# Performance work log

Measured on AMD Instinct MI355X. Metric: run time of the kernel, lower is better.

## Reference

```python
import jax, jax.numpy as jnp
import numpy as np

B, N_PER, C, KG, KTOP, KNN = 8, 2048, 256, 16, 512, 32
N = B * N_PER
E = N * KG
EPS = 1e-5


def setup_inputs() -> dict:
    key = jax.random.key(0)
    ks = jax.random.split(key, 32)
    s = 0.05
    x = jax.random.normal(ks[0], (N, C), jnp.float32)
    x_origin = jax.random.normal(ks[1], (N, C), jnp.float32)
    xyz = jax.random.uniform(ks[2], (N, 3), jnp.float32)
    # graph: every node is a dst with KG incoming edges from random nodes of the SAME sample
    edge_dst = jnp.repeat(jnp.arange(N, dtype=jnp.int32), KG)
    src_local = jax.random.randint(ks[3], (E,), 0, N_PER, dtype=jnp.int32)
    edge_src = src_local + (edge_dst // N_PER) * N_PER
    # EdgeConv params (theta on x_j - x_i, phi on x_i)
    theta_w = jax.random.normal(ks[4], (C, C), jnp.float32) * s
    theta_b = jax.random.normal(ks[5], (C,), jnp.float32) * s
    phi_w = jax.random.normal(ks[6], (C, C), jnp.float32) * s
    phi_b = jax.random.normal(ks[7], (C,), jnp.float32) * s
    # region_score_mlp: Conv1d(C,64,1)-ReLU-BN(64)-Conv1d(64,32,1)-ReLU-BN(32)-Conv1d(32,1,1)
    w1 = jax.random.normal(ks[8], (64, C), jnp.float32) * s
    b1 = jax.random.normal(ks[9], (64,), jnp.float32) * s
    g1 = 1.0 + 0.1 * jax.random.normal(ks[10], (64,), jnp.float32)
    be1 = 0.1 * jax.random.normal(ks[11], (64,), jnp.float32)
    m1 = 0.1 * jax.random.normal(ks[12], (64,), jnp.float32)
    v1 = jax.random.uniform(ks[13], (64,), jnp.float32, 0.5, 1.5)
    w2 = jax.random.normal(ks[14], (32, 64), jnp.float32) * s
    b2 = jax.random.normal(ks[15], (32,), jnp.float32) * s
    g2 = 1.0 + 0.1 * jax.random.normal(ks[16], (32,), jnp.float32)
    be2 = 0.1 * jax.random.normal(ks[17], (32,), jnp.float32)
    m2 = 0.1 * jax.random.normal(ks[18], (32,), jnp.float32)
    v2 = jax.random.uniform(ks[19], (32,), jnp.float32, 0.5, 1.5)
    w3 = jax.random.normal(ks[20], (1, 32), jnp.float32) * s
    b3 = jax.random.normal(ks[21], (1,), jnp.float32) * s
    return dict(x=x, x_origin=x_origin, xyz=xyz, edge_src=edge_src, edge_dst=edge_dst,
                theta_w=theta_w, theta_b=theta_b, phi_w=phi_w, phi_b=phi_b,
                w1=w1, b1=b1, g1=g1, be1=be1, m1=m1, v1=v1,
                w2=w2, b2=b2, g2=g2, be2=be2, m2=m2, v2=v2, w3=w3, b3=b3)


def _bn(t, g, b, m, v):
    return (t - m) * jax.lax.rsqrt(v + EPS) * g + b


def _forward(x, x_origin, xyz, edge_src, edge_dst,
             theta_w, theta_b, phi_w, phi_b,
             w1, b1, g1, be1, m1, v1, w2, b2, g2, be2, m2, v2, w3, b3):
    # EdgeConv: h_i = max_{j->i}( theta(x_j - x_i) + phi(x_i) ), then residual add
    msg = ((x[edge_src] - x[edge_dst]) @ theta_w.T + theta_b
           + x[edge_dst] @ phi_w.T + phi_b)                      # [E, C]
    h = jax.ops.segment_max(msg, edge_dst, num_segments=N)       # [N, C]
    x1 = h + x                                                   # residual
    # per-node MLP (Conv1d kernel-size 1 == linear), BN in eval mode
    t = _bn(jax.nn.relu(x1 @ w1.T + b1), g1, be1, m1, v1)
    t = _bn(jax.nn.relu(t @ w2.T + b2), g2, be2, m2, v2)
    score = t @ w3.T + b3                                        # [N, 1]
    score_b = score.reshape(B, N_PER)                            # vps_score
    # per-batch top-k (cls=False path: select by raw score, descending)
    topk_vals, topk_idx = jax.lax.top_k(score_b, KTOP)           # [B, KTOP]
    perm = (topk_idx + jnp.arange(B, dtype=topk_idx.dtype)[:, None] * N_PER).reshape(-1)
    x_new = x1[perm].reshape(B, KTOP, C)
    x_copy = x_origin[perm].reshape(B, KTOP, -1)
    xyz_sel = xyz[perm].reshape(B, KTOP, 3)
    # rebuild 32-NN graph per sample on selected points (batched, no per-b python calls)
    d2 = jnp.sum((xyz_sel[:, :, None, :] - xyz_sel[:, None, :, :]) ** 2, axis=-1)  # [B,K,K]
    _, knn_idx = jax.lax.top_k(-d2, KNN)                         # [B, KTOP, 32]
    return knn_idx, x_new, x_copy, score_b, topk_vals


def reference(x, x_origin, xyz, edge_src, edge_dst,
              theta_w, theta_b, phi_w, phi_b,
              w1, b1, g1, be1, m1, v1, w2, b2, g2, be2, m2, v2, w3, b3):
    return _forward(x, x_origin, xyz, edge_src, edge_dst,
                    theta_w, theta_b, phi_w, phi_b,
                    w1, b1, g1, be1, m1, v1, w2, b2, g2, be2, m2, v2, w3, b3)
```

## Files before the change

kernel.cpp:

```cpp
#include <hip/hip_runtime.h>
#include <math.h>

constexpr int B     = 8;
constexpr int N_PER = 2048;
constexpr int C     = 256;
constexpr int KG    = 16;
constexpr int KTOP  = 512;
constexpr int KNN   = 32;
constexpr int N     = B * N_PER;
constexpr float EPS = 1e-5f;

typedef __attribute__((ext_vector_type(8))) short  short8;
typedef __attribute__((ext_vector_type(4))) float  f32x4;

__device__ inline void split3(float f, unsigned short& h, unsigned short& m,
                              unsigned short& l)
{
    const unsigned u  = __float_as_uint(f);
    const unsigned r1 = (u + 0x7FFFu + ((u >> 16) & 1u)) & 0xFFFF0000u;
    h = (unsigned short)(r1 >> 16);
    const float f2 = f - __uint_as_float(r1);
    const unsigned u2 = __float_as_uint(f2);
    const unsigned r2 = (u2 + 0x7FFFu + ((u2 >> 16) & 1u)) & 0xFFFF0000u;
    m = (unsigned short)(r2 >> 16);
    const float f3 = f2 - __uint_as_float(r2);
    const unsigned u3 = __float_as_uint(f3);
    l = (unsigned short)((u3 + 0x7FFFu + ((u3 >> 16) & 1u)) >> 16);
}

__device__ inline void cvt_store24(unsigned short* dh, unsigned short* dm,
                                   unsigned short* dl, float4 a, float4 b)
{
    short8 h, m, l;
    unsigned short hh, mm, ll;
    float v[8] = {a.x, a.y, a.z, a.w, b.x, b.y, b.z, b.w};
#pragma unroll
    for (int j = 0; j < 8; ++j) {
        split3(v[j], hh, mm, ll);
        h[j] = (short)hh;
        m[j] = (short)mm;
        l[j] = (short)ll;
    }
    *(short8*)dh = h;
    *(short8*)dm = m;
    *(short8*)dl = l;
}

__device__ inline void split8v(const float* __restrict__ s,
                               unsigned short* __restrict__ dh,
                               unsigned short* __restrict__ dm,
                               unsigned short* __restrict__ dl)
{
    float4 a = *(const float4*)s;
    float4 b = *(const float4*)(s + 4);
    float v[8] = {a.x, a.y, a.z, a.w, b.x, b.y, b.z, b.w};
    short8 h8, m8, l8;
    unsigned short hh, mm, ll;
#pragma unroll
    for (int j = 0; j < 8; ++j) {
        split3(v[j], hh, mm, ll);
        h8[j] = (short)hh;
        m8[j] = (short)mm;
        l8[j] = (short)ll;
    }
    *(short8*)dh = h8;
    *(short8*)dm = m8;
    *(short8*)dl = l8;
}

constexpr int GW = C * C / 8;

__global__ __launch_bounds__(256) void k0w_split(
    const float* __restrict__ thw, const float* __restrict__ phw,
    unsigned short* __restrict__ th, unsigned short* __restrict__ tm,
    unsigned short* __restrict__ tl,
    unsigned short* __restrict__ ph, unsigned short* __restrict__ pm,
    unsigned short* __restrict__ pl)
{
    const int g = blockIdx.x * 256 + threadIdx.x;
    if (g < GW) {
        const int o = g * 8;
        split8v(thw + o, th + o, tm + o, tl + o);
    } else if (g < 2 * GW) {
        const int o = (g - GW) * 8;
        split8v(phw + o, ph + o, pm + o, pl + o);
    }
}

__global__ __launch_bounds__(256) void k1_wp(
    const float* __restrict__ x,
    const unsigned short* __restrict__ th, const unsigned short* __restrict__ tm,
    const unsigned short* __restrict__ tl,
    const unsigned short* __restrict__ ph, const unsigned short* __restrict__ pm,
    const unsigned short* __restrict__ pl,
    const float* __restrict__ thb, const float* __restrict__ phb,
    float* __restrict__ T, float* __restrict__ R)
{
    constexpr int BM = 128, BN = 64, ST = 40;
    __shared__ unsigned short sA[3][BM * ST];
    __shared__ unsigned short sT[3][BN * ST];
    __shared__ unsigned short sP[3][BN * ST];

    const int tid  = threadIdx.x;
    const int row0 = blockIdx.x * BM;
    const int n0   = blockIdx.y * BN;
    const int lane = tid & 63;
    const int wv   = tid >> 6;
    const int wr   = (wv >> 1) * 64;
    const int wc   = (wv & 1) * 32;
    const int fr   = lane & 15;
    const int fk   = (lane >> 4) * 8;
    const int ar0  = tid >> 2;
    const int ac   = (tid & 3) * 8;

    f32x4 acTh[4][2], acTl[4][2], acQh[4][2], acQl[4][2];
    const f32x4 zz = {0.f, 0.f, 0.f, 0.f};
#pragma unroll
    for (int m = 0; m < 4; ++m)
#pragma unroll
        for (int n = 0; n < 2; ++n) {
            acTh[m][n] = zz; acTl[m][n] = zz;
            acQh[m][n] = zz; acQl[m][n] = zz;
        }

    const float* xA0 = x + (size_t)(row0 + ar0)      * C + ac;
    const float* xA1 = x + (size_t)(row0 + 64 + ar0) * C + ac;
    const size_t offW = (size_t)(n0 + ar0) * C + ac;

    float4 a0a = *(const float4*)(xA0 + 0), a0b = *(const float4*)(xA0 + 4);
    float4 a1a = *(const float4*)(xA1 + 0), a1b = *(const float4*)(xA1 + 4);
    short8 rTh = *(const short8*)(th + offW);
    short8 rTm = *(const short8*)(tm + offW);
    short8 rTl = *(const short8*)(tl + offW);
    short8 rPh = *(const short8*)(ph + offW);
    short8 rPm = *(const short8*)(pm + offW);
    short8 rPl = *(const short8*)(pl + offW);

    const int sOffA0 = ar0 * ST + ac;
    const int sOffA1 = (64 + ar0) * ST + ac;
    const int aBase  = (wr + fr) * ST + fk;
    const int bBase  = (wc + fr) * ST + fk;

    for (int step = 0; step < 8; ++step) {
        __syncthreads();
        cvt_store24(sA[0] + sOffA0, sA[1] + sOffA0, sA[2] + sOffA0, a0a, a0b);
        cvt_store24(sA[0] + sOffA1, sA[1] + sOffA1, sA[2] + sOffA1, a1a, a1b);
        *(short8*)(sT[0] + sOffA0) = rTh;
        *(short8*)(sT[1] + sOffA0) = rTm;
        *(short8*)(sT[2] + sOffA0) = rTl;
        *(short8*)(sP[0] + sOffA0) = rPh;
        *(short8*)(sP[1] + sOffA0) = rPm;
        *(short8*)(sP[2] + sOffA0) = rPl;
        __syncthreads();

        if (step < 7) {
            const int kn = (step + 1) * 32;
            a0a = *(const float4*)(xA0 + kn); a0b = *(const float4*)(xA0 + kn + 4);
            a1a = *(const float4*)(xA1 + kn); a1b = *(const float4*)(xA1 + kn + 4);
            rTh = *(const short8*)(th + offW + kn);
            rTm = *(const short8*)(tm + offW + kn);
            rTl = *(const short8*)(tl + offW + kn);
            rPh = *(const short8*)(ph + offW + kn);
            rPm = *(const short8*)(pm + offW + kn);
            rPl = *(const short8*)(pl + offW + kn);
        }

        short8 a1f[4], a2f[4], a3f[4];
#pragma unroll
        for (int m = 0; m < 4; ++m) {
            const int r = aBase + m * 16 * ST;
            a1f[m] = *(const short8*)(sA[0] + r);
            a2f[m] = *(const short8*)(sA[1] + r);
            a3f[m] = *(const short8*)(sA[2] + r);
        }
        {
            short8 t0[2], p0[2];
#pragma unroll
            for (int n = 0; n < 2; ++n) {
                const int r = bBase + n * 16 * ST;
                t0[n] = *(const short8*)(sT[0] + r);
                p0[n] = *(const short8*)(sP[0] + r);
            }
#pragma unroll
            for (int m = 0; m < 4; ++m)
#pragma unroll
                for (int n = 0; n < 2; ++n) {
                    acTh[m][n] = __builtin_amdgcn_mfma_f32_16x16x32_bf16(a1f[m], t0[n], acTh[m][n], 0, 0, 0);
                    acQh[m][n] = __builtin_amdgcn_mfma_f32_16x16x32_bf16(a1f[m], p0[n], acQh[m][n], 0, 0, 0);
                    acTl[m][n] = __builtin_amdgcn_mfma_f32_16x16x32_bf16(a2f[m], t0[n], acTl[m][n], 0, 0, 0);
                    acQl[m][n] = __builtin_amdgcn_mfma_f32_16x16x32_bf16(a2f[m], p0[n], acQl[m][n], 0, 0, 0);
                    acTl[m][n] = __builtin_amdgcn_mfma_f32_16x16x32_bf16(a3f[m], t0[n], acTl[m][n], 0, 0, 0);
                    acQl[m][n] = __builtin_amdgcn_mfma_f32_16x16x32_bf16(a3f[m], p0[n], acQl[m][n], 0, 0, 0);
                }
        }
        {
            short8 t1[2], p1[2];
#pragma unroll
            for (int n = 0; n < 2; ++n) {
                const int r = bBase + n * 16 * ST;
                t1[n] = *(const short8*)(sT[1] + r);
                p1[n] = *(const short8*)(sP[1] + r);
            }
#pragma unroll
            for (int m = 0; m < 4; ++m)
#pragma unroll
                for (int n = 0; n < 2; ++n) {
                    acTl[m][n] = __builtin_amdgcn_mfma_f32_16x16x32_bf16(a1f[m], t1[n], acTl[m][n], 0, 0, 0);
                    acQl[m][n] = __builtin_amdgcn_mfma_f32_16x16x32_bf16(a1f[m], p1[n], acQl[m][n], 0, 0, 0);
                    acTl[m][n] = __builtin_amdgcn_mfma_f32_16x16x32_bf16(a2f[m], t1[n], acTl[m][n], 0, 0, 0);
                    acQl[m][n] = __builtin_amdgcn_mfma_f32_16x16x32_bf16(a2f[m], p1[n], acQl[m][n], 0, 0, 0);
                }
        }
        {
            short8 t2[2], p2[2];
#pragma unroll
            for (int n = 0; n < 2; ++n) {
                const int r = bBase + n * 16 * ST;
                t2[n] = *(const short8*)(sT[2] + r);
                p2[n] = *(const short8*)(sP[2] + r);
            }
#pragma unroll
            for (int m = 0; m < 4; ++m)
#pragma unroll
                for (int n = 0; n < 2; ++n) {
                    acTl[m][n] = __builtin_amdgcn_mfma_f32_16x16x32_bf16(a1f[m], t2[n], acTl[m][n], 0, 0, 0);
                    acQl[m][n] = __builtin_amdgcn_mfma_f32_16x16x32_bf16(a1f[m], p2[n], acQl[m][n], 0, 0, 0);
                }
        }
    }

    const int cr = (lane >> 4) * 4;
#pragma unroll
    for (int m = 0; m < 4; ++m) {
#pragma unroll
        for (int n = 0; n < 2; ++n) {
            const int col  = n0 + wc + n * 16 + fr;
            const float bias = thb[col] + phb[col];
#pragma unroll
            for (int j = 0; j < 4; ++j) {
                const int row = row0 + wr + m * 16 + cr + j;
                const size_t off = (size_t)row * C + col;
                const float tval = acTh[m][n][j] + acTl[m][n][j];
                const float qval = acQh[m][n][j] + acQl[m][n][j];
                T[off] = tval;
                R[off] = x[off] + qval + bias - tval;
            }
        }
    }
}

__global__ __launch_bounds__(256) void k1_fb(
    const float* __restrict__ x, const float* __restrict__ thw,
    const float* __restrict__ phw, const float* __restrict__ thb,
    const float* __restrict__ phb, float* __restrict__ T, float* __restrict__ R)
{
    constexpr int BM = 128, BN = 64, ST = 40;
    __shared__ unsigned short sA[3][BM * ST];
    __shared__ unsigned short sT[3][BN * ST];
    __shared__ unsigned short sP[3][BN * ST];

    const int tid  = threadIdx.x;
    const int row0 = blockIdx.x * BM;
    const int n0   = blockIdx.y * BN;
    const int lane = tid & 63;
    const int wv   = tid >> 6;
    const int wr   = (wv >> 1) * 64;
    const int wc   = (wv & 1) * 32;
    const int fr   = lane & 15;
    const int fk   = (lane >> 4) * 8;
    const int ar0 = tid >> 2;
    const int ac  = (tid & 3) * 8;

    f32x4 acTh[4][2], acTl[4][2], acQh[4][2], acQl[4][2];
    const f32x4 zz = {0.f, 0.f, 0.f, 0.f};
#pragma unroll
    for (int m = 0; m < 4; ++m)
#pragma unroll
        for (int n = 0; n < 2; ++n) {
            acTh[m][n] = zz; acTl[m][n] = zz;
            acQh[m][n] = zz; acQl[m][n] = zz;
        }

    const float* xA0 = x   + (size_t)(row0 + ar0)      * C + ac;
    const float* xA1 = x   + (size_t)(row0 + 64 + ar0) * C + ac;
    const float* wT  = thw + (size_t)(n0 + ar0)        * C + ac;
    const float* wP  = phw + (size_t)(n0 + ar0)        * C + ac;

    float4 a0a = *(const float4*)(xA0 + 0), a0b = *(const float4*)(xA0 + 4);
    float4 a1a = *(const float4*)(xA1 + 0), a1b = *(const float4*)(xA1 + 4);
    float4 ta  = *(const float4*)(wT  + 0), tb_ = *(const float4*)(wT  + 4);
    float4 pa  = *(const float4*)(wP  + 0), pb_ = *(const float4*)(wP  + 4);

    const int sOffA0 = ar0 * ST + ac;
    const int sOffA1 = (64 + ar0) * ST + ac;
    const int aBase  = (wr + fr) * ST + fk;
    const int bBase  = (wc + fr) * ST + fk;

    for (int step = 0; step < 8; ++step) {
        __syncthreads();
        cvt_store24(sA[0] + sOffA0, sA[1] + sOffA0, sA[2] + sOffA0, a0a, a0b);
        cvt_store24(sA[0] + sOffA1, sA[1] + sOffA1, sA[2] + sOffA1, a1a, a1b);
        cvt_store24(sT[0] + sOffA0, sT[1] + sOffA0, sT[2] + sOffA0, ta,  tb_);
        cvt_store24(sP[0] + sOffA0, sP[1] + sOffA0, sP[2] + sOffA0, pa,  pb_);
        __syncthreads();

        if (step < 7) {
            const int kn = (step + 1) * 32;
            a0a = *(const float4*)(xA0 + kn); a0b = *(const float4*)(xA0 + kn + 4);
            a1a = *(const float4*)(xA1 + kn); a1b = *(const float4*)(xA1 + kn + 4);
            ta  = *(const float4*)(wT  + kn); tb_ = *(const float4*)(wT  + kn + 4);
            pa  = *(const float4*)(wP  + kn); pb_ = *(const float4*)(wP  + kn + 4);
        }

        short8 a1f[4], a2f[4], a3f[4];
#pragma unroll
        for (int m = 0; m < 4; ++m) {
            const int r = aBase + m * 16 * ST;
            a1f[m] = *(const short8*)(sA[0] + r);
            a2f[m] = *(const short8*)(sA[1] + r);
            a3f[m] = *(const short8*)(sA[2] + r);
        }
        {
            short8 t0[2], p0[2];
#pragma unroll
            for (int n = 0; n < 2; ++n) {
                const int r = bBase + n * 16 * ST;
                t0[n] = *(const short8*)(sT[0] + r);
                p0[n] = *(const short8*)(sP[0] + r);
            }
#pragma unroll
            for (int m = 0; m < 4; ++m)
#pragma unroll
                for (int n = 0; n < 2; ++n) {
                    acTh[m][n] = __builtin_amdgcn_mfma_f32_16x16x32_bf16(a1f[m], t0[n], acTh[m][n], 0, 0, 0);
                    acQh[m][n] = __builtin_amdgcn_mfma_f32_16x16x32_bf16(a1f[m], p0[n], acQh[m][n], 0, 0, 0);
                    acTl[m][n] = __builtin_amdgcn_mfma_f32_16x16x32_bf16(a2f[m], t0[n], acTl[m][n], 0, 0, 0);
                    acQl[m][n] = __builtin_amdgcn_mfma_f32_16x16x32_bf16(a2f[m], p0[n], acQl[m][n], 0, 0, 0);
                    acTl[m][n] = __builtin_amdgcn_mfma_f32_16x16x32_bf16(a3f[m], t0[n], acTl[m][n], 0, 0, 0);
                    acQl[m][n] = __builtin_amdgcn_mfma_f32_16x16x32_bf16(a3f[m], p0[n], acQl[m][n], 0, 0, 0);
                }
        }
        {
            short8 t1[2], p1[2];
#pragma unroll
            for (int n = 0; n < 2; ++n) {
                const int r = bBase + n * 16 * ST;
                t1[n] = *(const short8*)(sT[1] + r);
                p1[n] = *(const short8*)(sP[1] + r);
            }
#pragma unroll
            for (int m = 0; m < 4; ++m)
#pragma unroll
                for (int n = 0; n < 2; ++n) {
                    acTl[m][n] = __builtin_amdgcn_mfma_f32_16x16x32_bf16(a1f[m], t1[n], acTl[m][n], 0, 0, 0);
                    acQl[m][n] = __builtin_amdgcn_mfma_f32_16x16x32_bf16(a1f[m], p1[n], acQl[m][n], 0, 0, 0);
                    acTl[m][n] = __builtin_amdgcn_mfma_f32_16x16x32_bf16(a2f[m], t1[n], acTl[m][n], 0, 0, 0);
                    acQl[m][n] = __builtin_amdgcn_mfma_f32_16x16x32_bf16(a2f[m], p1[n], acQl[m][n], 0, 0, 0);
                }
        }
        {
            short8 t2[2], p2[2];
#pragma unroll
            for (int n = 0; n < 2; ++n) {
                const int r = bBase + n * 16 * ST;
                t2[n] = *(const short8*)(sT[2] + r);
                p2[n] = *(const short8*)(sP[2] + r);
            }
#pragma unroll
            for (int m = 0; m < 4; ++m)
#pragma unroll
                for (int n = 0; n < 2; ++n) {
                    acTl[m][n] = __builtin_amdgcn_mfma_f32_16x16x32_bf16(a1f[m], t2[n], acTl[m][n], 0, 0, 0);
                    acQl[m][n] = __builtin_amdgcn_mfma_f32_16x16x32_bf16(a1f[m], p2[n], acQl[m][n], 0, 0, 0);
                }
        }
    }

    const int cr = (lane >> 4) * 4;
#pragma unroll
    for (int m = 0; m < 4; ++m) {
#pragma unroll
        for (int n = 0; n < 2; ++n) {
            const int col  = n0 + wc + n * 16 + fr;
            const float bias = thb[col] + phb[col];
#pragma unroll
            for (int j = 0; j < 4; ++j) {
                const int row = row0 + wr + m * 16 + cr + j;
                const size_t off = (size_t)row * C + col;
                const float tval = acTh[m][n][j] + acTl[m][n][j];
                const float qval = acQh[m][n][j] + acQl[m][n][j];
                T[off] = tval;
                R[off] = x[off] + qval + bias - tval;
            }
        }
    }
}

__global__ __launch_bounds__(256) void k2a_gather_max(
    const int* __restrict__ esrc, const float* __restrict__ T, float* x1r)
{
    const int gb = blockIdx.x;
    const int b  = gb & 7;
    const int node0 = b * N_PER + (gb >> 3) * 4;
    const int t = threadIdx.x;
    __shared__ int s[4][KG];
    if (t < 64) s[t >> 4][t & 15] = esrc[(node0 + (t >> 4)) * KG + (t & 15)];
    __syncthreads();
    const int m  = t >> 6;
    const int c4 = (t & 63) * 4;
    float4 acc = make_float4(-INFINITY, -INFINITY, -INFINITY, -INFINITY);
#pragma unroll
    for (int k = 0; k < KG; ++k) {
        const float4 v = *(const float4*)&T[(size_t)s[m][k] * C + c4];
        acc.x = fmaxf(acc.x, v.x);  acc.y = fmaxf(acc.y, v.y);
        acc.z = fmaxf(acc.z, v.z);  acc.w = fmaxf(acc.w, v.w);
    }
    const size_t off = (size_t)(node0 + m) * C + c4;
    float4 r = *(const float4*)&x1r[off];
    r.x += acc.x;  r.y += acc.y;  r.z += acc.z;  r.w += acc.w;
    *(float4*)&x1r[off] = r;
}

__global__ __launch_bounds__(256) void k2bc_score(
    const float* __restrict__ x1, const float* __restrict__ w1,
    const float* __restrict__ b1, const float* __restrict__ g1,
    const float* __restrict__ be1, const float* __restrict__ m1,
    const float* __restrict__ v1,
    const float* __restrict__ w2, const float* __restrict__ b2,
    const float* __restrict__ g2, const float* __restrict__ be2,
    const float* __restrict__ m2, const float* __restrict__ v2,
    const float* __restrict__ w3, const float* __restrict__ b3,
    float* __restrict__ score_ws, float* __restrict__ out_score)
{
    constexpr int BK = 16, ST = 68;
    __shared__ float Xs[BK * ST];
    __shared__ float Ws[BK * ST];
    __shared__ float t1s[64 * 65];
    __shared__ float w2s[32 * 65];
    __shared__ float w3s[32];
    __shared__ float zs[64 * 33];
    const int tid  = threadIdx.x;
    const int row0 = blockIdx.x * 64;
    const int tx = tid & 15, ty = tid >> 4;
    const int lm = tid >> 2, lq = (tid & 3) << 2;

    float acc[4][4] = {{0.f}};
    for (int k0 = 0; k0 < C; k0 += BK) {
        float4 fx = *(const float4*)(x1 + (size_t)(row0 + lm) * C + k0 + lq);
        float4 fw = *(const float4*)(w1 + (size_t)lm * C + k0 + lq);
        __syncthreads();
        Xs[(lq + 0) * ST + lm] = fx.x;  Xs[(lq + 1) * ST + lm] = fx.y;
        Xs[(lq + 2) * ST + lm] = fx.z;  Xs[(lq + 3) * ST + lm] = fx.w;
        Ws[(lq + 0) * ST + lm] = fw.x;  Ws[(lq + 1) * ST + lm] = fw.y;
        Ws[(lq + 2) * ST + lm] = fw.z;  Ws[(lq + 3) * ST + lm] = fw.w;
        __syncthreads();
#pragma unroll
        for (int k = 0; k < BK; ++k) {
            float4 a4 = *(const float4*)&Xs[k * ST + (ty << 2)];
            float4 w4 = *(const float4*)&Ws[k * ST + (tx << 2)];
            float av[4] = {a4.x, a4.y, a4.z, a4.w};
            float wv[4] = {w4.x, w4.y, w4.z, w4.w};
#pragma unroll
            for (int i2 = 0; i2 < 4; ++i2)
#pragma unroll
                for (int j2 = 0; j2 < 4; ++j2) acc[i2][j2] += av[i2] * wv[j2];
        }
    }
    __syncthreads();
#pragma unroll
    for (int i2 = 0; i2 < 4; ++i2) {
        const int mrow = (ty << 2) + i2;
#pragma unroll
        for (int j2 = 0; j2 < 4; ++j2) {
            const int o = (tx << 2) + j2;
            float y = acc[i2][j2] + b1[o];
            y = fmaxf(y, 0.f);
            y = (y - m1[o]) * (1.0f / sqrtf(v1[o] + EPS)) * g1[o] + be1[o];
            t1s[mrow * 65 + o] = y;
        }
    }
    for (int idx = tid; idx < 2048; idx += 256)
        w2s[(idx >> 6) * 65 + (idx & 63)] = w2[idx];
    if (tid < 32) w3s[tid] = w3[tid];
    __syncthreads();

    const int o = tid & 31;
    const float inv2 = (1.0f / sqrtf(v2[o] + EPS)) * g2[o];
#pragma unroll
    for (int p = 0; p < 8; ++p) {
        const int nl = p * 8 + (tid >> 5);
        float z = 0.f;
#pragma unroll
        for (int j = 0; j < 64; ++j) z += t1s[nl * 65 + j] * w2s[o * 65 + j];
        z += b2[o];
        z = fmaxf(z, 0.f);
        z = (z - m2[o]) * inv2 + be2[o];
        zs[nl * 33 + o] = z;
    }
    __syncthreads();

    if (tid < 64) {
        float sacc = 0.f;
#pragma unroll
        for (int j = 0; j < 32; ++j) sacc += zs[tid * 33 + j] * w3s[j];
        sacc += b3[0];
        const int node = row0 + tid;
        score_ws[node]  = sacc;
        out_score[node] = sacc;
    }
}

__global__ __launch_bounds__(1024) void k3_topk(
    const float* __restrict__ score, const float* __restrict__ xyz,
    float* __restrict__ out_topk, int* __restrict__ perm,
    float* __restrict__ xsel)
{
    __shared__ unsigned long long keys[N_PER];
    const int b = blockIdx.x;
    const int t = threadIdx.x;
    for (int i = t; i < N_PER; i += 1024) {
        const float v = score[b * N_PER + i];
        unsigned u = __float_as_uint(v);
        const unsigned ua = (u & 0x80000000u) ? ~u : (u | 0x80000000u);
        const unsigned ud = ~ua;
        keys[i] = ((unsigned long long)ud << 32) | (unsigned)i;
    }
    __syncthreads();
    for (int k = 2; k <= N_PER; k <<= 1) {
        for (int j = k >> 1; j > 0; j >>= 1) {
            for (int i = t; i < N_PER; i += 1024) {
                const int ixj = i ^ j;
                if (ixj > i) {
                    const unsigned long long a = keys[i], c = keys[ixj];
                    const bool up = ((i & k) == 0);
                    if ((a > c) == up) { keys[i] = c; keys[ixj] = a; }
                }
            }
            __syncthreads();
        }
    }
    for (int r = t; r < KTOP; r += 1024) {
        const int idx = (int)(keys[r] & 0xffffffffu);
        const int g = b * N_PER + idx;
        out_topk[b * KTOP + r] = score[g];
        perm[b * KTOP + r] = g;
        xsel[(b * KTOP + r) * 3 + 0] = xyz[g * 3 + 0];
        xsel[(b * KTOP + r) * 3 + 1] = xyz[g * 3 + 1];
        xsel[(b * KTOP + r) * 3 + 2] = xyz[g * 3 + 2];
    }
}

__global__ __launch_bounds__(256) void k5_knn(
    const int* __restrict__ perm, const float* __restrict__ xsel,
    const float* __restrict__ x1, const float* __restrict__ xorig,
    float* __restrict__ out_xnew, float* __restrict__ out_xcopy,
    float* __restrict__ out_knn)
{
    constexpr int G = 4;
    __shared__ float px[KTOP], py[KTOP], pz[KTOP];
    __shared__ unsigned long long keys[G * KTOP];
    const int t  = threadIdx.x;
    const int q0 = blockIdx.x * G;
    const int b  = q0 >> 9;
    const int i0 = q0 & 511;

    for (int idx = t; idx < KTOP; idx += 256) {
        const size_t base = ((size_t)b * KTOP + idx) * 3;
        px[idx] = xsel[base + 0];
        py[idx] = xsel[base + 1];
        pz[idx] = xsel[base + 2];
    }
#pragma unroll
    for (int p = 0; p < G; ++p) {
        const int row = q0 + p;
        const int g = perm[row];
        out_xnew [(size_t)row * C + t] = x1   [(size_t)g * C + t];
        out_xcopy[(size_t)row * C + t] = xorig[(size_t)g * C + t];
    }
    __syncthreads();

    for (int w = t; w < G * KTOP; w += 256) {
        const int p = w >> 9, idx = w & 511;
        const float dx = __fsub_rn(px[i0 + p], px[idx]);
        const float dy = __fsub_rn(py[i0 + p], py[idx]);
        const float dz = __fsub_rn(pz[i0 + p], pz[idx]);
        const float d2 = __fadd_rn(__fadd_rn(__fmul_rn(dx, dx), __fmul_rn(dy, dy)),
                                   __fmul_rn(dz, dz));
        keys[w] = ((unsigned long long)__float_as_uint(d2) << 32) | (unsigned)idx;
    }
    __syncthreads();

    for (int k = 2; k <= 32; k <<= 1) {
        for (int j = k >> 1; j > 0; j >>= 1) {
            for (int i = t; i < G * KTOP; i += 256) {
                const int ixj = i ^ j;
                if (ixj > i) {
                    const int il = i & 31;
                    const unsigned long long a = keys[i], c = keys[ixj];
                    const bool up = ((il & k) == 0) || (k == 32);
                    if ((a > c) == up) { keys[i] = c; keys[ixj] = a; }
                }
            }
            __syncthreads();
        }
    }
    for (int r = 0; r < 4; ++r) {
        const int npairs = 8 >> r;
        const int total  = G * npairs * 32;
        for (int w = t; w < total; w += 256) {
            const int p  = w / (npairs * 32);
            const int rm = w - p * (npairs * 32);
            const int m  = rm >> 5, i = rm & 31;
            const int baseA = p * KTOP + m * (64 << r);
            const int baseB = baseA + (32 << r);
            const unsigned long long a = keys[baseA + i];
            const unsigned long long c = keys[baseB + 31 - i];
            keys[baseA + i] = (c < a) ? c : a;
        }
        __syncthreads();
        for (int j = 16; j > 0; j >>= 1) {
            for (int w = t; w < total; w += 256) {
                const int p  = w / (npairs * 32);
                const int rm = w - p * (npairs * 32);
                const int m  = rm >> 5, i = rm & 31;
                const int ixj = i ^ j;
                if (ixj > i) {
                    const int baseA = p * KTOP + m * (64 << r);
                    const unsigned long long a = keys[baseA + i], c = keys[baseA + ixj];
                    if (a > c) { keys[baseA + i] = c; keys[baseA + ixj] = a; }
                }
            }
            __syncthreads();
        }
    }

    if (t < G * KNN) {
        const int p = t >> 5, r = t & 31;
        out_knn[((size_t)(q0 + p)) * KNN + r] =
            (float)(unsigned)(keys[p * KTOP + r] & 0xffffffffu);
    }
}

extern "C" void kernel_launch(void* const* d_in, const int* in_sizes, int n_in,
                              void* d_out, int out_size, void* d_ws, size_t ws_size,
                              hipStream_t stream)
{
    const float* x     = (const float*)d_in[0];
    const float* xorig = (const float*)d_in[1];
    const float* xyz   = (const float*)d_in[2];
    const int*   esrc  = (const int*)d_in[3];
    const float* thw = (const float*)d_in[5];
    const float* thb = (const float*)d_in[6];
    const float* phw = (const float*)d_in[7];
    const float* phb = (const float*)d_in[8];
    const float* w1  = (const float*)d_in[9];
    const float* b1  = (const float*)d_in[10];
    const float* g1  = (const float*)d_in[11];
    const float* be1 = (const float*)d_in[12];
    const float* m1  = (const float*)d_in[13];
    const float* v1  = (const float*)d_in[14];
    const float* w2  = (const float*)d_in[15];
    const float* b2  = (const float*)d_in[16];
    const float* g2  = (const float*)d_in[17];
    const float* be2 = (const float*)d_in[18];
    const float* m2  = (const float*)d_in[19];
    const float* v2  = (const float*)d_in[20];
    const float* w3  = (const float*)d_in[21];
    const float* b3  = (const float*)d_in[22];

    float* ws   = (float*)d_ws;
    float* T    = ws;
    float* x1   = ws + (size_t)N * C;
    float* sc   = ws + 2 * (size_t)N * C;
    int*   perm = (int*)(sc + N);
    float* xsel = (float*)(perm + B * KTOP);

    unsigned short* th = (unsigned short*)(xsel + (size_t)B * KTOP * 3);
    unsigned short* tm = th + (size_t)C * C;
    unsigned short* tl = tm + (size_t)C * C;
    unsigned short* ph = tl + (size_t)C * C;
    unsigned short* pm = ph + (size_t)C * C;
    unsigned short* pl = pm + (size_t)C * C;
    const size_t ws_need = (size_t)((char*)(pl + (size_t)C * C) - (char*)ws);
    const bool planes_ok = (ws_size >= ws_need);

    float* out     = (float*)d_out;
    float* o_knn   = out;
    float* o_xnew  = o_knn + (size_t)B * KTOP * KNN;
    float* o_xcopy = o_xnew + (size_t)B * KTOP * C;
    float* o_score = o_xcopy + (size_t)B * KTOP * C;
    float* o_topk  = o_score + (size_t)B * N_PER;

    if (planes_ok) {
        k0w_split<<<(2 * GW + 255) / 256, 256, 0, stream>>>(
            thw, phw, th, tm, tl, ph, pm, pl);
        k1_wp<<<dim3(N / 128, C / 64), 256, 0, stream>>>(
            x, th, tm, tl, ph, pm, pl, thb, phb, T, x1);
    } else {
        k1_fb<<<dim3(N / 128, C / 64), 256, 0, stream>>>(x, thw, phw, thb, phb, T, x1);
    }
    k2a_gather_max<<<N / 4, 256, 0, stream>>>(esrc, T, x1);
    k2bc_score<<<N / 64, 256, 0, stream>>>(x1, w1, b1, g1, be1, m1, v1,
                                           w2, b2, g2, be2, m2, v2, w3, b3, sc, o_score);
    k3_topk<<<B, 1024, 0, stream>>>(sc, xyz, o_topk, perm, xsel);
    k5_knn<<<B * KTOP / 4, 256, 0, stream>>>(perm, xsel, x1, xorig,
                                             o_xnew, o_xcopy, o_knn);
}
```

Measured before the change: 255.3 us.

## Replace bitonic sorts with rank-counting top-k and wave-level kNN selection

The per-batch top-k bitonic sort ran on only 8 blocks of 1024 threads. It is replaced by a rank computation spread over 64 blocks: each thread counts how many keys are smaller than its own key and scatters its element directly if that rank is below KTOP. The kNN bitonic sort/merge in shared memory becomes a per-wave selection. Each lane sorts 8 candidates in registers, then 32 rounds of wave-wide shuffle min-reductions extract the nearest neighbours. This removes many __syncthreads barriers and shared-memory passes, at the cost of O(N^2) comparisons in the rank kernel, with each block redundantly reloading all keys of its batch.

```diff
diff --git a/kernel.cpp b/kernel.cpp
--- a/kernel.cpp
+++ b/kernel.cpp
@@ -510,15 +510,16 @@
     }
 }
 
-__global__ __launch_bounds__(1024) void k3_topk(
+__global__ __launch_bounds__(256) void k3_rank(
     const float* __restrict__ score, const float* __restrict__ xyz,
     float* __restrict__ out_topk, int* __restrict__ perm,
     float* __restrict__ xsel)
 {
     __shared__ unsigned long long keys[N_PER];
-    const int b = blockIdx.x;
-    const int t = threadIdx.x;
-    for (int i = t; i < N_PER; i += 1024) {
+    const int b   = blockIdx.x >> 3;
+    const int seg = blockIdx.x & 7;
+    const int t   = threadIdx.x;
+    for (int i = t; i < N_PER; i += 256) {
         const float v = score[b * N_PER + i];
         unsigned u = __float_as_uint(v);
         const unsigned ua = (u & 0x80000000u) ? ~u : (u | 0x80000000u);
@@ -526,31 +527,31 @@
         keys[i] = ((unsigned long long)ud << 32) | (unsigned)i;
     }
     __syncthreads();
-    for (int k = 2; k <= N_PER; k <<= 1) {
-        for (int j = k >> 1; j > 0; j >>= 1) {
-            for (int i = t; i < N_PER; i += 1024) {
-                const int ixj = i ^ j;
-                if (ixj > i) {
-                    const unsigned long long a = keys[i], c = keys[ixj];
-                    const bool up = ((i & k) == 0);
-                    if ((a > c) == up) { keys[i] = c; keys[ixj] = a; }
-                }
-            }
-            __syncthreads();
-        }
-    }
-    for (int r = t; r < KTOP; r += 1024) {
-        const int idx = (int)(keys[r] & 0xffffffffu);
-        const int g = b * N_PER + idx;
-        out_topk[b * KTOP + r] = score[g];
-        perm[b * KTOP + r] = g;
-        xsel[(b * KTOP + r) * 3 + 0] = xyz[g * 3 + 0];
-        xsel[(b * KTOP + r) * 3 + 1] = xyz[g * 3 + 1];
-        xsel[(b * KTOP + r) * 3 + 2] = xyz[g * 3 + 2];
-    }
-}
-
-__global__ __launch_bounds__(256) void k5_knn(
+    const int i = seg * 256 + t;
+    const unsigned long long k = keys[i];
+    int r = 0;
+#pragma unroll 8
+    for (int j = 0; j < N_PER; ++j) r += (keys[j] < k) ? 1 : 0;
+    if (r < KTOP) {
+        const int g = b * N_PER + i;
+        const int o = b * KTOP + r;
+        out_topk[o] = score[g];
+        perm[o] = g;
+        xsel[o * 3 + 0] = xyz[g * 3 + 0];
+        xsel[o * 3 + 1] = xyz[g * 3 + 1];
+        xsel[o * 3 + 2] = xyz[g * 3 + 2];
+    }
+}
+
+__device__ inline unsigned long long shfl_xor_u64(unsigned long long v, int m)
+{
+    unsigned lo = (unsigned)v, hi = (unsigned)(v >> 32);
+    lo = __shfl_xor(lo, m, 64);
+    hi = __shfl_xor(hi, m, 64);
+    return ((unsigned long long)hi << 32) | lo;
+}
+
+__global__ __launch_bounds__(256) void k5_rank(
     const int* __restrict__ perm, const float* __restrict__ xsel,
     const float* __restrict__ x1, const float* __restrict__ xorig,
     float* __restrict__ out_xnew, float* __restrict__ out_xcopy,
@@ -558,7 +559,6 @@
 {
     constexpr int G = 4;
     __shared__ float px[KTOP], py[KTOP], pz[KTOP];
-    __shared__ unsigned long long keys[G * KTOP];
     const int t  = threadIdx.x;
     const int q0 = blockIdx.x * G;
     const int b  = q0 >> 9;
@@ -579,65 +579,46 @@
     }
     __syncthreads();
 
-    for (int w = t; w < G * KTOP; w += 256) {
-        const int p = w >> 9, idx = w & 511;
-        const float dx = __fsub_rn(px[i0 + p], px[idx]);
-        const float dy = __fsub_rn(py[i0 + p], py[idx]);
-        const float dz = __fsub_rn(pz[i0 + p], pz[idx]);
+    const int w    = t >> 6;
+    const int lane = t & 63;
+    const int q    = i0 + w;
+    const float qx = px[q], qy = py[q], qz = pz[q];
+
+    unsigned long long arr[8];
+#pragma unroll
+    for (int e = 0; e < 8; ++e) {
+        const int j = lane + 64 * e;
+        const float dx = __fsub_rn(qx, px[j]);
+        const float dy = __fsub_rn(qy, py[j]);
+        const float dz = __fsub_rn(qz, pz[j]);
         const float d2 = __fadd_rn(__fadd_rn(__fmul_rn(dx, dx), __fmul_rn(dy, dy)),
                                    __fmul_rn(dz, dz));
-        keys[w] = ((unsigned long long)__float_as_uint(d2) << 32) | (unsigned)idx;
-    }
-    __syncthreads();
-
-    for (int k = 2; k <= 32; k <<= 1) {
-        for (int j = k >> 1; j > 0; j >>= 1) {
-            for (int i = t; i < G * KTOP; i += 256) {
-                const int ixj = i ^ j;
-                if (ixj > i) {
-                    const int il = i & 31;
-                    const unsigned long long a = keys[i], c = keys[ixj];
-                    const bool up = ((il & k) == 0) || (k == 32);
-                    if ((a > c) == up) { keys[i] = c; keys[ixj] = a; }
-                }
-            }
-            __syncthreads();
-        }
-    }
-    for (int r = 0; r < 4; ++r) {
-        const int npairs = 8 >> r;
-        const int total  = G * npairs * 32;
-        for (int w = t; w < total; w += 256) {
-            const int p  = w / (npairs * 32);
-            const int rm = w - p * (npairs * 32);
-            const int m  = rm >> 5, i = rm & 31;
-            const int baseA = p * KTOP + m * (64 << r);
-            const int baseB = baseA + (32 << r);
-            const unsigned long long a = keys[baseA + i];
-            const unsigned long long c = keys[baseB + 31 - i];
-            keys[baseA + i] = (c < a) ? c : a;
-        }
-        __syncthreads();
-        for (int j = 16; j > 0; j >>= 1) {
-            for (int w = t; w < total; w += 256) {
-                const int p  = w / (npairs * 32);
-                const int rm = w - p * (npairs * 32);
-                const int m  = rm >> 5, i = rm & 31;
-                const int ixj = i ^ j;
-                if (ixj > i) {
-                    const int baseA = p * KTOP + m * (64 << r);
-                    const unsigned long long a = keys[baseA + i], c = keys[baseA + ixj];
-                    if (a > c) { keys[baseA + i] = c; keys[baseA + ixj] = a; }
-                }
-            }
-            __syncthreads();
-        }
-    }
-
-    if (t < G * KNN) {
-        const int p = t >> 5, r = t & 31;
-        out_knn[((size_t)(q0 + p)) * KNN + r] =
-            (float)(unsigned)(keys[p * KTOP + r] & 0xffffffffu);
+        arr[e] = ((unsigned long long)__float_as_uint(d2) << 32) | (unsigned)j;
+    }
+#pragma unroll
+    for (int pass = 0; pass < 7; ++pass)
+#pragma unroll
+        for (int i = 0; i < 7; ++i) {
+            if (i < 7 - pass) {
+                const unsigned long long a = arr[i], c = arr[i + 1];
+                arr[i]     = (a < c) ? a : c;
+                arr[i + 1] = (a < c) ? c : a;
+            }
+        }
+    float* dst = out_knn + (size_t)(q0 + w) * KNN;
+    for (int r = 0; r < KNN; ++r) {
+        unsigned long long m = arr[0];
+#pragma unroll
+        for (int off = 32; off; off >>= 1) {
+            const unsigned long long o = shfl_xor_u64(m, off);
+            m = (o < m) ? o : m;
+        }
+        if (arr[0] == m) {
+            dst[r] = (float)(unsigned)(m & 0xffffffffu);
+#pragma unroll
+            for (int i = 0; i < 7; ++i) arr[i] = arr[i + 1];
+            arr[7] = ~0ull;
+        }
     }
 }
 
@@ -702,7 +683,7 @@
     k2a_gather_max<<<N / 4, 256, 0, stream>>>(esrc, T, x1);
     k2bc_score<<<N / 64, 256, 0, stream>>>(x1, w1, b1, g1, be1, m1, v1,
                                            w2, b2, g2, be2, m2, v2, w3, b3, sc, o_score);
-    k3_topk<<<B, 1024, 0, stream>>>(sc, xyz, o_topk, perm, xsel);
-    k5_knn<<<B * KTOP / 4, 256, 0, stream>>>(perm, xsel, x1, xorig,
-                                             o_xnew, o_xcopy, o_knn);
-}
+    k3_rank<<<8 * B, 256, 0, stream>>>(sc, xyz, o_topk, perm, xsel);
+    k5_rank<<<B * KTOP / 4, 256, 0, stream>>>(perm, xsel, x1, xorig,
+                                              o_xnew, o_xcopy, o_knn);
+}
```

After: 250.3 us. About the same (-1.9%).
